# Optimization experiments

Hardware: AMD Instinct MI355X
Metric: run time of the kernel (lower is better)

Reference implementation:

```python
import jax, jax.numpy as jnp
import numpy as np

B, S, HID = 2, 2048, 2048
NH, NKV, HD = 16, 4, 128
MAXPOS = 2048


def _rope_tables(features, length, max_timescale=10000.0):
    fraction = jnp.arange(0, features, 2, dtype=jnp.float32) / features
    inv_freq = 1.0 / (max_timescale ** fraction)
    sinusoid = jnp.einsum('i,j->ij', jnp.arange(length, dtype=jnp.float32), inv_freq)
    sinusoid = jnp.concatenate([sinusoid, sinusoid], axis=-1)  # [length, features]
    return jnp.sin(sinusoid), jnp.cos(sinusoid)


def rotate_half(x):
    x1, x2 = jnp.split(x, 2, axis=-1)
    return jnp.concatenate([-x2, x1], axis=-1)


def setup_inputs() -> dict:
    key = jax.random.key(0)
    k1, k2, k3, k4, k5 = jax.random.split(key, 5)
    scale = 1.0 / np.sqrt(HID)
    hidden_states = jax.random.normal(k1, (B, S, HID), dtype=jnp.float32)
    Wq = jax.random.normal(k2, (NH * HD, HID), dtype=jnp.float32) * scale
    Wk = jax.random.normal(k3, (NKV * HD, HID), dtype=jnp.float32) * scale
    Wv = jax.random.normal(k4, (NKV * HD, HID), dtype=jnp.float32) * scale
    Wo = jax.random.normal(k5, (HID, NH * HD), dtype=jnp.float32) * scale
    # causal additive mask [B,1,S,S]
    neg = jnp.finfo(jnp.float32).min
    causal = jnp.where(jnp.tril(jnp.ones((S, S), dtype=bool)), 0.0, neg)
    attention_mask = jnp.broadcast_to(causal[None, None], (B, 1, S, S))
    sin, cos = _rope_tables(HD, MAXPOS)
    return {"hidden_states": hidden_states, "attention_mask": attention_mask,
            "Wq": Wq, "Wk": Wk, "Wv": Wv, "Wo": Wo, "sin": sin, "cos": cos}


def reference(hidden_states, attention_mask, Wq, Wk, Wv, Wo, sin, cos):
    bsz, qlen, _ = hidden_states.shape
    # projections (Linear, no bias): x @ W.T -> [B,S,heads,hd]
    q = (hidden_states @ Wq.T).reshape(bsz, qlen, NH, HD)
    k = (hidden_states @ Wk.T).reshape(bsz, qlen, NKV, HD)
    v = (hidden_states @ Wv.T).reshape(bsz, qlen, NKV, HD)
    # rotary embedding (applied in [B,S,H,D] layout)
    qcos = cos[:qlen][None, :, None, :]
    qsin = sin[:qlen][None, :, None, :]
    q = q * qcos + rotate_half(q) * qsin
    k = k * qcos + rotate_half(k) * qsin
    # GQA: repeat_kv equivalent via einsum grouping; expand kv heads to NH
    n_rep = NH // NKV
    q_g = q.reshape(bsz, qlen, NKV, n_rep, HD)  # group queries per kv head
    # scores: NOTE original applies no 1/sqrt(d) scaling
    scores = jnp.einsum('bqhrd,bkhd->bhrqk', q_g, k).reshape(bsz, NH, qlen, qlen)
    mask = attention_mask.at[:, :, :, 0].set(0.0)
    scores = scores + mask
    probs = jax.nn.softmax(scores.astype(jnp.float32), axis=-1).astype(q.dtype)
    probs_g = probs.reshape(bsz, NKV, n_rep, qlen, qlen)
    out = jnp.einsum('bhrqk,bkhd->bqhrd', probs_g, v).reshape(bsz, qlen, NH * HD)
    return out @ Wo.T
```

## Files before the change

### kernel.cpp

```cpp
#include <hip/hip_runtime.h>
#include <hip/hip_bf16.h>

typedef _Float16 f16x8 __attribute__((ext_vector_type(8)));
typedef __fp16 h16x2 __attribute__((ext_vector_type(2)));
typedef float f32x4 __attribute__((ext_vector_type(4)));
typedef float f32x16 __attribute__((ext_vector_type(16)));

#define B_    2
#define S_    2048
#define HID_  2048
#define NH_   16
#define NKV_  4
#define HD_   128
#define M_TOK 4096
#define NQKV  3072

#define MFMA16(a, b, c) __builtin_amdgcn_mfma_f32_16x16x32_f16(a, b, c, 0, 0, 0)
#define MFMA32(a, b, c) __builtin_amdgcn_mfma_f32_32x32x16_f16(a, b, c, 0, 0, 0)

union UW { unsigned u; h16x2 h; };

__device__ __forceinline__ unsigned short f2h(float f) {
  _Float16 h = (_Float16)f;
  return *(unsigned short*)&h;
}

__device__ __forceinline__ void gload_lds16(const unsigned short* g, unsigned short* l) {
  __builtin_amdgcn_global_load_lds((const __attribute__((address_space(1))) void*)g,
                                   (__attribute__((address_space(3))) void*)l,
                                   16, 0, 0);
}

__global__ void cast_f32_f16(const float* __restrict__ src, unsigned short* __restrict__ dst, int n4) {
  int i = blockIdx.x * blockDim.x + threadIdx.x;
  int stride = gridDim.x * blockDim.x;
  for (int idx = i; idx < n4; idx += stride) {
    float4 v = reinterpret_cast<const float4*>(src)[idx];
    ushort4 o;
    o.x = f2h(v.x); o.y = f2h(v.y); o.z = f2h(v.z); o.w = f2h(v.w);
    reinterpret_cast<ushort4*>(dst)[idx] = o;
  }
}

__global__ void cast_weights(const float* __restrict__ Wq, const float* __restrict__ Wk,
                             const float* __restrict__ Wv, const float* __restrict__ Wo,
                             unsigned short* __restrict__ dst) {
  const int n1 = 2048 * 2048 / 4, n2 = 512 * 2048 / 4;
  const int ntot = n1 * 2 + n2 * 2;
  int i = blockIdx.x * blockDim.x + threadIdx.x;
  int stride = gridDim.x * blockDim.x;
  for (int idx = i; idx < ntot; idx += stride) {
    const float* src; int off;
    if (idx < n1)                { src = Wq; off = idx; }
    else if (idx < n1 + n2)      { src = Wk; off = idx - n1; }
    else if (idx < n1 + 2 * n2)  { src = Wv; off = idx - n1 - n2; }
    else                         { src = Wo; off = idx - n1 - 2 * n2; }
    float4 v = reinterpret_cast<const float4*>(src)[off];
    ushort4 o;
    o.x = f2h(v.x); o.y = f2h(v.y); o.z = f2h(v.z); o.w = f2h(v.w);
    reinterpret_cast<ushort4*>(dst)[idx] = o;
  }
}

#define BM 128
#define BN 128
#define BK 32

template <bool OUT16>
__global__ __launch_bounds__(256) void gemm_bt_f16(
    const unsigned short* __restrict__ A, const unsigned short* __restrict__ Bm,
    void* __restrict__ Cv, int M, int N, int K) {
  __shared__ unsigned short As[BM * BK];
  __shared__ unsigned short Bs[BN * BK];
  const int tid  = threadIdx.x;
  const int lane = tid & 63;
  const int wave = tid >> 6;
  const int nbn  = N / BN;
  const int brow = (blockIdx.x / nbn) * BM;
  const int bcol = (blockIdx.x % nbn) * BN;
  const int wr = (wave >> 1) * 64;
  const int wc = (wave & 1) * 64;

  const int srow = wave * 16 + (lane >> 2);
  const int scol = (lane & 3) * 8;
  const unsigned short* ag = A + (size_t)(brow + srow) * K + scol;
  const unsigned short* bg = Bm + (size_t)(bcol + srow) * K + scol;
  unsigned short* aldsw = As + wave * 512;
  unsigned short* bldsw = Bs + wave * 512;

  f32x4 acc[4][4];
#pragma unroll
  for (int m = 0; m < 4; ++m)
#pragma unroll
    for (int n = 0; n < 4; ++n) acc[m][n] = (f32x4){0.f, 0.f, 0.f, 0.f};

  const int lr = lane & 15;
  const int lg = lane >> 4;

  for (int kt = 0; kt < K; kt += BK) {
    __syncthreads();
    gload_lds16(ag + kt, aldsw);
    gload_lds16(ag + (size_t)64 * K + kt, aldsw + 2048);
    gload_lds16(bg + kt, bldsw);
    gload_lds16(bg + (size_t)64 * K + kt, bldsw + 2048);
    __syncthreads();
    f16x8 af[4], bfr[4];
#pragma unroll
    for (int m = 0; m < 4; ++m)
      af[m] = *reinterpret_cast<const f16x8*>(&As[(wr + m * 16 + lr) * BK + lg * 8]);
#pragma unroll
    for (int n = 0; n < 4; ++n)
      bfr[n] = *reinterpret_cast<const f16x8*>(&Bs[(wc + n * 16 + lr) * BK + lg * 8]);
#pragma unroll
    for (int m = 0; m < 4; ++m)
#pragma unroll
      for (int n = 0; n < 4; ++n)
        acc[m][n] = MFMA16(af[m], bfr[n], acc[m][n]);
  }

#pragma unroll
  for (int m = 0; m < 4; ++m) {
#pragma unroll
    for (int r = 0; r < 4; ++r) {
      int row = brow + wr + m * 16 + lg * 4 + r;
      if (OUT16) {
        unsigned short* cp = (unsigned short*)Cv + (size_t)row * N + bcol + wc + lr;
#pragma unroll
        for (int n = 0; n < 4; ++n) cp[n * 16] = f2h(acc[m][n][r]);
      } else {
        float* cp = (float*)Cv + (size_t)row * N + bcol + wc + lr;
#pragma unroll
        for (int n = 0; n < 4; ++n) cp[n * 16] = acc[m][n][r];
      }
    }
  }
}

__global__ void rope_relayout(const unsigned short* __restrict__ QKV,
                              const float* __restrict__ sin_t, const float* __restrict__ cos_t,
                              unsigned short* __restrict__ Qo, unsigned short* __restrict__ Ko,
                              unsigned short* __restrict__ Vt) {
  int idx = blockIdx.x * blockDim.x + threadIdx.x;
  int d  = idx & 63;
  int t  = idx >> 6;
  int hh = t % 24;
  int bs = t / 24;
  int s  = bs & (S_ - 1);
  int b  = bs >> 11;
  const _Float16* xrow = (const _Float16*)QKV + (size_t)bs * NQKV;
  if (hh < 16) {
    float x0 = (float)xrow[hh * 128 + d], x1 = (float)xrow[hh * 128 + 64 + d];
    float c = cos_t[s * 128 + d], sn = sin_t[s * 128 + d];
    unsigned short* qp = Qo + (((size_t)(b * 16 + hh) * S_) + s) * 128 + d;
    qp[0]  = f2h(x0 * c - x1 * sn);
    qp[64] = f2h(x1 * c + x0 * sn);
  } else if (hh < 20) {
    int kvh = hh - 16;
    float x0 = (float)xrow[2048 + kvh * 128 + d], x1 = (float)xrow[2048 + kvh * 128 + 64 + d];
    float c = cos_t[s * 128 + d], sn = sin_t[s * 128 + d];
    unsigned short* kp = Ko + (((size_t)(b * 4 + kvh) * S_) + s) * 128 + d;
    kp[0]  = f2h(x0 * c - x1 * sn);
    kp[64] = f2h(x1 * c + x0 * sn);
  } else {
    int kvh = hh - 20;
    unsigned short x0 = QKV[(size_t)bs * NQKV + 2560 + kvh * 128 + d];
    unsigned short x1 = QKV[(size_t)bs * NQKV + 2560 + kvh * 128 + 64 + d];
    unsigned short* vp = Vt + ((size_t)(b * 4 + kvh) * 128 + d) * S_ + s;
    vp[0]        = x0;
    vp[64 * S_]  = x1;
  }
}

__global__ __launch_bounds__(256, 2) void flash_attn6(
    const unsigned short* __restrict__ Q, const unsigned short* __restrict__ Kk,
    const unsigned short* __restrict__ Vt, unsigned short* __restrict__ Ao) {
  __shared__ _Float16 Kl[2][64 * 128];
  __shared__ _Float16 Vl[2][128 * 64];
  const int lane = threadIdx.x & 63;
  const int w    = threadIdx.x >> 6;
  const int bh   = blockIdx.x & 31;
  const int j    = (int)(blockIdx.x >> 5);
  const int bq   = (j < 8) ? (15 - j) : (j - 8);
  const int b    = bh >> 4, h = bh & 15, kvh = h >> 2;
  const int q31  = lane & 31;
  const int hi   = lane >> 5;
  const int qb   = bq * 128;
  const int wqb  = qb + w * 32;
  const int qrow = wqb + q31;

  const _Float16* Qp = (const _Float16*)Q + (((size_t)(b * 16 + h) * S_) + qrow) * 128;
  const _Float16* Kp = (const _Float16*)Kk + ((size_t)(b * 4 + kvh) * S_) * 128;
  const _Float16* Vp = (const _Float16*)Vt + ((size_t)(b * 4 + kvh) * 128) * S_;

  f16x8 qf[8];
#pragma unroll
  for (int s = 0; s < 8; ++s) {
    f16x8 t = *reinterpret_cast<const f16x8*>(Qp + s * 16 + hi * 8);
#pragma unroll
    for (int jj = 0; jj < 8; ++jj) t[jj] = (_Float16)((float)t[jj] * 1.44269504f);
    qf[s] = t;
  }

  f32x16 po0 = {}, po1 = {}, po2 = {}, po3 = {};
  float m = -1e30f, l = 0.f;

  const int krow = (lane >> 4);
  const int vrow = (lane >> 3);
  const int wklim = wqb + 32;
  const int nt = qb / 64 + 2;

#define STAGE(K0S, BUF)                                                               \
  {                                                                                   \
    unsigned short* kdst = (unsigned short*)Kl[BUF] + w * 2048;                       \
    unsigned short* vdst = (unsigned short*)Vl[BUF] + w * 2048;                       \
    _Pragma("unroll") for (int jj = 0; jj < 4; ++jj) {                                \
      const int jx = w * 4 + jj;                                                      \
      const int kr = jx * 4 + krow;                                                   \
      const int kc = (lane & 15) ^ (kr & 7);                                          \
      gload_lds16((const unsigned short*)(Kp + (size_t)((K0S) + kr) * 128 + kc * 8),  \
                  kdst + jj * 512);                                                   \
      const int vr = jx * 8 + vrow;                                                   \
      const int vc = (lane & 7) ^ (vr & 7);                                           \
      gload_lds16((const unsigned short*)(Vp + (size_t)vr * S_ + (K0S) + vc * 8),     \
                  vdst + jj * 512);                                                   \
    }                                                                                 \
  }

  STAGE(0, 0)
  __syncthreads();

  int cur = 0;
  const int r7 = q31 & 7;
  for (int t = 0; t < nt; ++t) {
    const int k0 = t * 64;
    if (t + 1 < nt) STAGE((t + 1) * 64, cur ^ 1)

    if (k0 < wklim) {
      f32x16 s0 = {}, s1 = {};
      const _Float16* Kc = Kl[cur];
      __builtin_amdgcn_s_setprio(1);
#pragma unroll
      for (int s = 0; s < 8; ++s) {
        const int cc = (hi + 2 * s) ^ r7;
        f16x8 kf0 = *reinterpret_cast<const f16x8*>(Kc + q31 * 128 + cc * 8);
        f16x8 kf1 = *reinterpret_cast<const f16x8*>(Kc + (q31 + 32) * 128 + cc * 8);
        s0 = MFMA32(kf0, qf[s], s0);
        s1 = MFMA32(kf1, qf[s], s1);
      }
      __builtin_amdgcn_s_setprio(0);

      if (k0 + 63 > wqb) {
        int qrel = qrow - k0 - 4 * hi;
#pragma unroll
        for (int r = 0; r < 16; ++r) {
          int cr = (r & 3) + 8 * (r >> 2);
          if (cr > qrel)      s0[r] = -1e30f;
          if (cr + 32 > qrel) s1[r] = -1e30f;
        }
      }
      float tmx[8];
#pragma unroll
      for (int r = 0; r < 8; ++r)
        tmx[r] = fmaxf(fmaxf(s0[r], s0[r + 8]), fmaxf(s1[r], s1[r + 8]));
#pragma unroll
      for (int d = 4; d > 0; d >>= 1)
#pragma unroll
        for (int r = 0; r < d; ++r) tmx[r] = fmaxf(tmx[r], tmx[r + d]);
      float pmax = fmaxf(tmx[0], __shfl_xor(tmx[0], 32));
      if (__any(pmax > m + 8.0f)) {
        float mn = fmaxf(m, pmax);
        float sc = __builtin_amdgcn_exp2f(m - mn);
        l *= sc;
#pragma unroll
        for (int r = 0; r < 16; ++r) {
          po0[r] *= sc; po1[r] *= sc; po2[r] *= sc; po3[r] *= sc;
        }
        m = mn;
      }
#pragma unroll
      for (int r = 0; r < 16; ++r) s0[r] = __builtin_amdgcn_exp2f(s0[r] - m);
#pragma unroll
      for (int r = 0; r < 16; ++r) s1[r] = __builtin_amdgcn_exp2f(s1[r] - m);
      float u[8];
#pragma unroll
      for (int r = 0; r < 8; ++r)
        u[r] = (s0[r] + s0[r + 8]) + (s1[r] + s1[r + 8]);
#pragma unroll
      for (int d = 4; d > 0; d >>= 1)
#pragma unroll
        for (int r = 0; r < d; ++r) u[r] += u[r + d];
      l += u[0] + __shfl_xor(u[0], 32);

      f16x8 pa[4];
#pragma unroll
      for (int sl = 0; sl < 4; ++sl) {
        f32x16 sv = (sl < 2) ? s0 : s1;
        const int R = (sl & 1) * 8;
        UW w00, w01, w10, w11;
        w00.h = __builtin_amdgcn_cvt_pkrtz(sv[R + 0], sv[R + 1]);
        w01.h = __builtin_amdgcn_cvt_pkrtz(sv[R + 2], sv[R + 3]);
        w10.h = __builtin_amdgcn_cvt_pkrtz(sv[R + 4], sv[R + 5]);
        w11.h = __builtin_amdgcn_cvt_pkrtz(sv[R + 6], sv[R + 7]);
        unsigned x00 = __shfl_xor(w00.u, 32);
        unsigned x01 = __shfl_xor(w01.u, 32);
        unsigned x10 = __shfl_xor(w10.u, 32);
        unsigned x11 = __shfl_xor(w11.u, 32);
        UW W0, W1, W2, W3;
        W0.u = hi ? x10 : w00.u;
        W1.u = hi ? x11 : w01.u;
        W2.u = hi ? w10.u : x00;
        W3.u = hi ? w11.u : x01;
        union { unsigned uu[4]; f16x8 v; } pk;
        pk.uu[0] = W0.u; pk.uu[1] = W1.u; pk.uu[2] = W2.u; pk.uu[3] = W3.u;
        pa[sl] = pk.v;
      }

      const _Float16* Vc = Vl[cur];
      __builtin_amdgcn_s_setprio(1);
#pragma unroll
      for (int s = 0; s < 4; ++s) {
        const int cc = (hi + 2 * s) ^ r7;
        f16x8 vf0 = *reinterpret_cast<const f16x8*>(Vc + q31 * 64 + cc * 8);
        po0 = MFMA32(vf0, pa[s], po0);
        f16x8 vf1 = *reinterpret_cast<const f16x8*>(Vc + (q31 + 32) * 64 + cc * 8);
        po1 = MFMA32(vf1, pa[s], po1);
        f16x8 vf2 = *reinterpret_cast<const f16x8*>(Vc + (q31 + 64) * 64 + cc * 8);
        po2 = MFMA32(vf2, pa[s], po2);
        f16x8 vf3 = *reinterpret_cast<const f16x8*>(Vc + (q31 + 96) * 64 + cc * 8);
        po3 = MFMA32(vf3, pa[s], po3);
      }
      __builtin_amdgcn_s_setprio(0);
    }

    __syncthreads();
    cur ^= 1;
  }
#undef STAGE

  float inv = 1.0f / l;
  unsigned short* orow = Ao + ((size_t)(b * S_ + qrow)) * 2048 + h * 128;
#define STORE_DB(PO, DB)                                                          \
  {                                                                               \
    _Pragma("unroll") for (int a4 = 0; a4 < 4; ++a4) {                            \
      UW e0, e1;                                                                  \
      e0.h = __builtin_amdgcn_cvt_pkrtz(PO[4 * a4 + 0] * inv, PO[4 * a4 + 1] * inv); \
      e1.h = __builtin_amdgcn_cvt_pkrtz(PO[4 * a4 + 2] * inv, PO[4 * a4 + 3] * inv); \
      unsigned long long pv = ((unsigned long long)e1.u << 32) | e0.u;            \
      *reinterpret_cast<unsigned long long*>(orow + DB * 32 + a4 * 8 + hi * 4) = pv; \
    }                                                                             \
  }
  STORE_DB(po0, 0)
  STORE_DB(po1, 1)
  STORE_DB(po2, 2)
  STORE_DB(po3, 3)
#undef STORE_DB
}

extern "C" void kernel_launch(void* const* d_in, const int* in_sizes, int n_in,
                              void* d_out, int out_size, void* d_ws, size_t ws_size,
                              hipStream_t stream) {
  const float* hs    = (const float*)d_in[0];
  const float* Wq    = (const float*)d_in[2];
  const float* Wk    = (const float*)d_in[3];
  const float* Wv    = (const float*)d_in[4];
  const float* Wo    = (const float*)d_in[5];
  const float* sin_t = (const float*)d_in[6];
  const float* cos_t = (const float*)d_in[7];

  char* ws = (char*)d_ws;
  unsigned short* Xb    = (unsigned short*)ws; ws += (size_t)M_TOK * HID_ * 2;
  unsigned short* Wqkvb = (unsigned short*)ws; ws += (size_t)NQKV * HID_ * 2;
  unsigned short* Wob   = (unsigned short*)ws; ws += (size_t)HID_ * HID_ * 2;
  unsigned short* QKV   = (unsigned short*)ws; ws += (size_t)M_TOK * NQKV * 2;
  unsigned short* Qb    = (unsigned short*)ws; ws += (size_t)B_ * NH_ * S_ * HD_ * 2;
  unsigned short* Kb    = (unsigned short*)ws; ws += (size_t)B_ * NKV_ * S_ * HD_ * 2;
  unsigned short* Vtb   = (unsigned short*)ws; ws += (size_t)B_ * NKV_ * S_ * HD_ * 2;
  unsigned short* Aob   = (unsigned short*)ws; ws += (size_t)M_TOK * HID_ * 2;

  cast_f32_f16<<<2048, 256, 0, stream>>>(hs, Xb, M_TOK * HID_ / 4);
  cast_weights<<<2048, 256, 0, stream>>>(Wq, Wk, Wv, Wo, Wqkvb);

  gemm_bt_f16<true><<<(M_TOK / BM) * (NQKV / BN), 256, 0, stream>>>(Xb, Wqkvb, QKV, M_TOK, NQKV, HID_);

  rope_relayout<<<(B_ * S_ * 24 * 64) / 256, 256, 0, stream>>>(QKV, sin_t, cos_t, Qb, Kb, Vtb);

  flash_attn6<<<512, 256, 0, stream>>>(Qb, Kb, Vtb, Aob);

  gemm_bt_f16<false><<<(M_TOK / BM) * (HID_ / BN), 256, 0, stream>>>(Aob, Wob, d_out, M_TOK, HID_, HID_);
}
```

Baseline: 249.6 us.

## Switch GEMM to 32x32x16 MFMA with XOR-swizzled LDS and reorder attention blocks

Rewrites the projection GEMM to use 32x32x16 MFMA tiles (2x2 per wave) instead of 16x16x32 tiles. Global-to-LDS loads get an XOR swizzle on the k-group, and the fragment reads undo it, to cut LDS bank conflicts. Larger MFMA tiles halve the per-wave fragment loads for the same math, at the cost of a scattered epilogue store pattern. The flash attention block order changes from interleaved to plain heaviest-first causal query blocks.

```diff
diff --git a/kernel.cpp b/kernel.cpp
--- a/kernel.cpp
+++ b/kernel.cpp
@@ -67,7 +67,7 @@
 #define BK 32
 
 template <bool OUT16>
-__global__ __launch_bounds__(256) void gemm_bt_f16(
+__global__ __launch_bounds__(256) void gemm_bt32(
     const unsigned short* __restrict__ A, const unsigned short* __restrict__ Bm,
     void* __restrict__ Cv, int M, int N, int K) {
   __shared__ unsigned short As[BM * BK];
@@ -80,22 +80,21 @@
   const int bcol = (blockIdx.x % nbn) * BN;
   const int wr = (wave >> 1) * 64;
   const int wc = (wave & 1) * 64;
+  const int l31 = lane & 31;
+  const int hi  = lane >> 5;
 
   const int srow = wave * 16 + (lane >> 2);
-  const int scol = (lane & 3) * 8;
-  const unsigned short* ag = A + (size_t)(brow + srow) * K + scol;
-  const unsigned short* bg = Bm + (size_t)(bcol + srow) * K + scol;
+  const int sg   = ((lane & 3) ^ ((lane >> 2) & 3)) * 8;
+  const unsigned short* ag = A + (size_t)(brow + srow) * K + sg;
+  const unsigned short* bg = Bm + (size_t)(bcol + srow) * K + sg;
   unsigned short* aldsw = As + wave * 512;
   unsigned short* bldsw = Bs + wave * 512;
 
-  f32x4 acc[4][4];
-#pragma unroll
-  for (int m = 0; m < 4; ++m)
-#pragma unroll
-    for (int n = 0; n < 4; ++n) acc[m][n] = (f32x4){0.f, 0.f, 0.f, 0.f};
-
-  const int lr = lane & 15;
-  const int lg = lane >> 4;
+  f32x16 acc[2][2];
+#pragma unroll
+  for (int mt = 0; mt < 2; ++mt)
+#pragma unroll
+    for (int nt = 0; nt < 2; ++nt) acc[mt][nt] = (f32x16){};
 
   for (int kt = 0; kt < K; kt += BK) {
     __syncthreads();
@@ -104,33 +103,42 @@
     gload_lds16(bg + kt, bldsw);
     gload_lds16(bg + (size_t)64 * K + kt, bldsw + 2048);
     __syncthreads();
-    f16x8 af[4], bfr[4];
-#pragma unroll
-    for (int m = 0; m < 4; ++m)
-      af[m] = *reinterpret_cast<const f16x8*>(&As[(wr + m * 16 + lr) * BK + lg * 8]);
-#pragma unroll
-    for (int n = 0; n < 4; ++n)
-      bfr[n] = *reinterpret_cast<const f16x8*>(&Bs[(wc + n * 16 + lr) * BK + lg * 8]);
-#pragma unroll
-    for (int m = 0; m < 4; ++m)
-#pragma unroll
-      for (int n = 0; n < 4; ++n)
-        acc[m][n] = MFMA16(af[m], bfr[n], acc[m][n]);
-  }
-
-#pragma unroll
-  for (int m = 0; m < 4; ++m) {
-#pragma unroll
-    for (int r = 0; r < 4; ++r) {
-      int row = brow + wr + m * 16 + lg * 4 + r;
-      if (OUT16) {
-        unsigned short* cp = (unsigned short*)Cv + (size_t)row * N + bcol + wc + lr;
-#pragma unroll
-        for (int n = 0; n < 4; ++n) cp[n * 16] = f2h(acc[m][n][r]);
-      } else {
-        float* cp = (float*)Cv + (size_t)row * N + bcol + wc + lr;
-#pragma unroll
-        for (int n = 0; n < 4; ++n) cp[n * 16] = acc[m][n][r];
+    f16x8 af[2][2], bf[2][2];
+#pragma unroll
+    for (int mt = 0; mt < 2; ++mt)
+#pragma unroll
+      for (int ks = 0; ks < 2; ++ks) {
+        const int row = wr + mt * 32 + l31;
+        const int g = (ks * 2 + hi) ^ (l31 & 3);
+        af[mt][ks] = *reinterpret_cast<const f16x8*>(&As[row * BK + g * 8]);
+      }
+#pragma unroll
+    for (int nt = 0; nt < 2; ++nt)
+#pragma unroll
+      for (int ks = 0; ks < 2; ++ks) {
+        const int row = wc + nt * 32 + l31;
+        const int g = (ks * 2 + hi) ^ (l31 & 3);
+        bf[nt][ks] = *reinterpret_cast<const f16x8*>(&Bs[row * BK + g * 8]);
+      }
+#pragma unroll
+    for (int ks = 0; ks < 2; ++ks)
+#pragma unroll
+      for (int mt = 0; mt < 2; ++mt)
+#pragma unroll
+        for (int nt = 0; nt < 2; ++nt)
+          acc[mt][nt] = MFMA32(af[mt][ks], bf[nt][ks], acc[mt][nt]);
+  }
+
+#pragma unroll
+  for (int mt = 0; mt < 2; ++mt) {
+#pragma unroll
+    for (int nt = 0; nt < 2; ++nt) {
+#pragma unroll
+      for (int r = 0; r < 16; ++r) {
+        const int row = brow + wr + mt * 32 + (r & 3) + 8 * (r >> 2) + 4 * hi;
+        const int col = bcol + wc + nt * 32 + l31;
+        if (OUT16) ((unsigned short*)Cv)[(size_t)row * N + col] = f2h(acc[mt][nt][r]);
+        else       ((float*)Cv)[(size_t)row * N + col] = acc[mt][nt][r];
       }
     }
   }
@@ -179,8 +187,7 @@
   const int lane = threadIdx.x & 63;
   const int w    = threadIdx.x >> 6;
   const int bh   = blockIdx.x & 31;
-  const int j    = (int)(blockIdx.x >> 5);
-  const int bq   = (j < 8) ? (15 - j) : (j - 8);
+  const int bq   = 15 - (int)(blockIdx.x >> 5);
   const int b    = bh >> 4, h = bh & 15, kvh = h >> 2;
   const int q31  = lane & 31;
   const int hi   = lane >> 5;
@@ -380,11 +387,11 @@
   cast_f32_f16<<<2048, 256, 0, stream>>>(hs, Xb, M_TOK * HID_ / 4);
   cast_weights<<<2048, 256, 0, stream>>>(Wq, Wk, Wv, Wo, Wqkvb);
 
-  gemm_bt_f16<true><<<(M_TOK / BM) * (NQKV / BN), 256, 0, stream>>>(Xb, Wqkvb, QKV, M_TOK, NQKV, HID_);
+  gemm_bt32<true><<<(M_TOK / BM) * (NQKV / BN), 256, 0, stream>>>(Xb, Wqkvb, QKV, M_TOK, NQKV, HID_);
 
   rope_relayout<<<(B_ * S_ * 24 * 64) / 256, 256, 0, stream>>>(QKV, sin_t, cos_t, Qb, Kb, Vtb);
 
   flash_attn6<<<512, 256, 0, stream>>>(Qb, Kb, Vtb, Aob);
 
-  gemm_bt_f16<false><<<(M_TOK / BM) * (HID_ / BN), 256, 0, stream>>>(Aob, Wob, d_out, M_TOK, HID_, HID_);
-}
+  gemm_bt32<false><<<(M_TOK / BM) * (HID_ / BN), 256, 0, stream>>>(Aob, Wob, d_out, M_TOK, HID_, HID_);
+}
```

After: 246.1 us (median of 2 runs). No clear change (-1.4%).
